# Optimization experiments

Measured on AMD Instinct MI355X. Metric: run time of the kernel, lower is better.

Reference implementation:

```python
import jax, jax.numpy as jnp
import numpy as np

IN_DIM = 768
HID = 128
NUM_CLASSES = 32
N_NODES = 50000
N_EDGES = 1600000


def setup_inputs() -> dict:
    key = jax.random.key(0)
    ks = jax.random.split(key, 8)
    x = jax.random.normal(ks[0], (N_NODES, IN_DIM), dtype=jnp.float32)
    edge_index = jax.random.randint(ks[1], (2, N_EDGES), 0, N_NODES, dtype=jnp.int64)
    # GCNConv weights (PyG: linear without bias inside propagate, bias added after aggregation)
    W1 = jax.random.normal(ks[2], (IN_DIM, HID), dtype=jnp.float32) / np.sqrt(IN_DIM)
    b1 = jnp.zeros((HID,), dtype=jnp.float32)
    W2 = jax.random.normal(ks[3], (HID, HID), dtype=jnp.float32) / np.sqrt(HID)
    b2 = jnp.zeros((HID,), dtype=jnp.float32)
    Wfc = jax.random.normal(ks[4], (HID, NUM_CLASSES), dtype=jnp.float32) / np.sqrt(HID)
    bfc = jnp.zeros((NUM_CLASSES,), dtype=jnp.float32)
    return {"x": x, "edge_index": edge_index, "W1": W1, "b1": b1,
            "W2": W2, "b2": b2, "Wfc": Wfc, "bfc": bfc}


def _gcn_conv(x, src, dst, norm, W, b, num_nodes):
    # PyG GCNConv: h = x @ W; out[i] = sum_j norm_ij * h[j]; out += b
    h = x @ W                      # [N, out_dim]
    msgs = h[src] * norm[:, None]  # gather + scale, [E+N, out_dim]
    out = jax.ops.segment_sum(msgs, dst, num_segments=num_nodes)
    return out + b


def reference(x, edge_index, W1, b1, W2, b2, Wfc, bfc):
    n = x.shape[0]
    loop = jnp.arange(n, dtype=edge_index.dtype)
    src = jnp.concatenate([edge_index[0], loop])  # add self-loops
    dst = jnp.concatenate([edge_index[1], loop])
    # symmetric normalization: deg computed on destination with unit edge weights
    deg = jax.ops.segment_sum(jnp.ones_like(src, dtype=x.dtype), dst, num_segments=n)
    dinv = jnp.where(deg > 0, jax.lax.rsqrt(jnp.maximum(deg, 1.0)), 0.0)
    norm = dinv[src] * dinv[dst]  # [E+N]

    h = jax.nn.relu(_gcn_conv(x, src, dst, norm, W1, b1, n))
    h = jax.nn.relu(_gcn_conv(h, src, dst, norm, W2, b2, n))
    return h @ Wfc + bfc
```

## Files before the change

kernel.cpp:

```cpp
#include <hip/hip_runtime.h>
#include <hip/hip_bf16.h>
#include <hip/hip_fp16.h>

#define N_NODES 50000
#define IN_DIM 768
#define HID 128
#define NCLS 32
#define CHUNK 8192
#define NBUCK ((N_NODES + 255) >> 8)

typedef __attribute__((ext_vector_type(8))) short bf16x8;
typedef __attribute__((ext_vector_type(4))) float f32x4;
typedef __attribute__((ext_vector_type(4))) unsigned short u16x4;

__device__ inline void split_bf16(float x, unsigned short& hi, unsigned short& lo) {
    unsigned int u = __float_as_uint(x);
    hi = (unsigned short)(u >> 16);
    float r = x - __uint_as_float(u & 0xFFFF0000u);
    lo = (unsigned short)(__float_as_uint(r) >> 16);
}

__global__ __launch_bounds__(256) void count_bucket(const int* __restrict__ raw, int E,
                                                    int* __restrict__ hist) {
    __shared__ int cnt[NBUCK];
    bool is64 = (raw[1] == 0 && raw[3] == 0 && raw[5] == 0 && raw[7] == 0);
    int t = threadIdx.x, b = blockIdx.x;
    if (t < NBUCK) cnt[t] = 0;
    __syncthreads();
    int base = b * CHUNK;
#pragma unroll
    for (int j = 0; j < CHUNK / 256; ++j) {
        int e = base + j * 256 + t;
        if (e < E) {
            int d = is64 ? raw[2 * (E + e)] : raw[E + e];
            atomicAdd(&cnt[d >> 8], 1);
        }
    }
    __syncthreads();
    if (t < NBUCK) hist[b * NBUCK + t] = cnt[t];
}

__global__ __launch_bounds__(256) void scan_off2(const int* __restrict__ hist, int nblk,
                                                 int E, int* __restrict__ bstart,
                                                 int* __restrict__ off) {
    __shared__ int tot[256];
    int t = threadIdx.x;
    int sum = 0;
    if (t < NBUCK)
        for (int b = 0; b < nblk; ++b) sum += hist[b * NBUCK + t];
    tot[t] = (t < NBUCK) ? sum : 0;
    __syncthreads();
    for (int o = 1; o < 256; o <<= 1) {
        int v = (t >= o) ? tot[t - o] : 0;
        __syncthreads();
        tot[t] += v;
        __syncthreads();
    }
    int excl = (t == 0) ? 0 : tot[t - 1];
    if (t < NBUCK) {
        bstart[t] = excl;
        int run = excl;
        for (int b = 0; b < nblk; ++b) {
            off[b * NBUCK + t] = run;
            run += hist[b * NBUCK + t];
        }
    }
    if (t == 0) bstart[NBUCK] = E;
}

__global__ __launch_bounds__(256) void chunk_scatter(const int* __restrict__ raw, int E,
                                                     const int* __restrict__ off,
                                                     unsigned int* __restrict__ ebuf) {
    __shared__ int offl[NBUCK];
    __shared__ int cnt[NBUCK];
    bool is64 = (raw[1] == 0 && raw[3] == 0 && raw[5] == 0 && raw[7] == 0);
    int t = threadIdx.x, b = blockIdx.x;
    if (t < NBUCK) { offl[t] = off[b * NBUCK + t]; cnt[t] = 0; }
    __syncthreads();
    int base = b * CHUNK;
#pragma unroll
    for (int j = 0; j < CHUNK / 256; ++j) {
        int e = base + j * 256 + t;
        if (e < E) {
            int s, d;
            if (is64) { s = raw[2 * e]; d = raw[2 * (E + e)]; }
            else      { s = raw[e];     d = raw[E + e]; }
            int k = d >> 8;
            int r = atomicAdd(&cnt[k], 1);
            ebuf[offl[k] + r] = ((unsigned int)(d & 255) << 16) | (unsigned int)s;
        }
    }
}

__global__ __launch_bounds__(256) void bucket_fine2(const unsigned int* __restrict__ ebuf,
                                                    const int* __restrict__ bstart,
                                                    int* __restrict__ rowp,
                                                    float* __restrict__ dinv,
                                                    unsigned short* __restrict__ csr,
                                                    int n, int E) {
    __shared__ int cnt[256];
    __shared__ int pre[256];
    __shared__ int fil[256];
    int k = blockIdx.x, t = threadIdx.x;
    int base = k << 8;
    int nn = min(256, n - base);
    int es = bstart[k], ee = bstart[k + 1];
    cnt[t] = 0;
    __syncthreads();
    for (int p = es + t; p < ee; p += 256) atomicAdd(&cnt[ebuf[p] >> 16], 1);
    __syncthreads();
    pre[t] = cnt[t];
    __syncthreads();
    for (int o = 1; o < 256; o <<= 1) {
        int v = (t >= o) ? pre[t - o] : 0;
        __syncthreads();
        pre[t] += v;
        __syncthreads();
    }
    int excl = (t == 0) ? 0 : pre[t - 1];
    if (t < nn) {
        rowp[base + t] = es + excl;
        dinv[base + t] = rsqrtf((float)(cnt[t] + 1));
    }
    if (k == gridDim.x - 1 && t == 0) rowp[n] = E;
    fil[t] = es + excl;
    __syncthreads();
    for (int p = es + t; p < ee; p += 256) {
        unsigned int u = ebuf[p];
        int q = atomicAdd(&fil[u >> 16], 1);
        csr[q] = (unsigned short)(u & 0xFFFFu);
    }
}

__global__ void pack_w(const float* __restrict__ W, int K,
                       unsigned short* __restrict__ ph, unsigned short* __restrict__ pl) {
    int gid = blockIdx.x * 256 + threadIdx.x;
    int total = (K / 32) * 8 * 64;
    if (gid >= total) return;
    int l = gid & 63;
    int c0 = (gid >> 6) & 7;
    int t = gid >> 9;
    int col = c0 * 16 + (l & 15);
    int k0 = t * 32 + ((l >> 4) << 3);
    size_t base = (size_t)gid * 8;
#pragma unroll
    for (int j = 0; j < 8; ++j) {
        unsigned short h, lo;
        split_bf16(W[(size_t)(k0 + j) * 128 + col], h, lo);
        ph[base + j] = h;
        pl[base + j] = lo;
    }
}

template <bool AHALF>
__device__ inline float4 loadA4(const void* A, size_t idx) {
    if constexpr (AHALF) {
        uint2 u = *(const uint2*)((const __half*)A + idx);
        float2 f0 = __half22float2(*(__half2*)&u.x);
        float2 f1 = __half22float2(*(__half2*)&u.y);
        return make_float4(f0.x, f0.y, f1.x, f1.y);
    } else {
        return *(const float4*)((const float*)A + idx);
    }
}

template <int K, bool AHALF>
__global__ __launch_bounds__(256) void gemm_mfma2(const void* __restrict__ A,
                                                  const unsigned short* __restrict__ Bph,
                                                  const unsigned short* __restrict__ Bpl,
                                                  const float* __restrict__ dinv,
                                                  __half* __restrict__ Chalf, int M) {
    __shared__ unsigned short Ah[64][40];
    __shared__ unsigned short Al[64][40];
    int tid = threadIdx.x;
    int wid = tid >> 6, lane = tid & 63;
    int wr = wid >> 1, wc = wid & 1;
    int row0 = blockIdx.x * 64;
    int lrow = lane & 15, lk = (lane >> 4) * 8;
    const int T = K / 32;

    int sidx0 = tid, sidx1 = 256 + tid;
    int sr0 = sidx0 >> 3, sc0 = (sidx0 & 7) * 4;
    int sr1 = sidx1 >> 3, sc1 = (sidx1 & 7) * 4;
    bool v0 = (row0 + sr0) < M, v1 = (row0 + sr1) < M;
    size_t ai0 = (size_t)(row0 + sr0) * K + sc0;
    size_t ai1 = (size_t)(row0 + sr1) * K + sc1;

    float4 pre0 = make_float4(0.f, 0.f, 0.f, 0.f), pre1 = pre0;
    if (v0) pre0 = loadA4<AHALF>(A, ai0);
    if (v1) pre1 = loadA4<AHALF>(A, ai1);

    f32x4 acc[2][4] = {};
    for (int t = 0; t < T; ++t) {
        u16x4 h, lo;
        split_bf16(pre0.x, ((unsigned short*)&h)[0], ((unsigned short*)&lo)[0]);
        split_bf16(pre0.y, ((unsigned short*)&h)[1], ((unsigned short*)&lo)[1]);
        split_bf16(pre0.z, ((unsigned short*)&h)[2], ((unsigned short*)&lo)[2]);
        split_bf16(pre0.w, ((unsigned short*)&h)[3], ((unsigned short*)&lo)[3]);
        *(u16x4*)&Ah[sr0][sc0] = h;
        *(u16x4*)&Al[sr0][sc0] = lo;
        split_bf16(pre1.x, ((unsigned short*)&h)[0], ((unsigned short*)&lo)[0]);
        split_bf16(pre1.y, ((unsigned short*)&h)[1], ((unsigned short*)&lo)[1]);
        split_bf16(pre1.z, ((unsigned short*)&h)[2], ((unsigned short*)&lo)[2]);
        split_bf16(pre1.w, ((unsigned short*)&h)[3], ((unsigned short*)&lo)[3]);
        *(u16x4*)&Ah[sr1][sc1] = h;
        *(u16x4*)&Al[sr1][sc1] = lo;
        __syncthreads();
        if (t + 1 < T) {
            pre0 = make_float4(0.f, 0.f, 0.f, 0.f); pre1 = pre0;
            if (v0) pre0 = loadA4<AHALF>(A, ai0 + (size_t)(t + 1) * 32);
            if (v1) pre1 = loadA4<AHALF>(A, ai1 + (size_t)(t + 1) * 32);
        }
        bf16x8 ah[2], al[2];
#pragma unroll
        for (int m = 0; m < 2; ++m) {
            int r = wr * 32 + m * 16 + lrow;
            ah[m] = *(const bf16x8*)&Ah[r][lk];
            al[m] = *(const bf16x8*)&Al[r][lk];
        }
        bf16x8 bh[4], bl[4];
#pragma unroll
        for (int n = 0; n < 4; ++n) {
            size_t boff = ((size_t)(t * 8 + wc * 4 + n) * 64 + lane) * 8;
            bh[n] = *(const bf16x8*)&Bph[boff];
            bl[n] = *(const bf16x8*)&Bpl[boff];
        }
#pragma unroll
        for (int m = 0; m < 2; ++m)
#pragma unroll
            for (int n = 0; n < 4; ++n) {
                acc[m][n] = __builtin_amdgcn_mfma_f32_16x16x32_bf16(ah[m], bh[n], acc[m][n], 0, 0, 0);
                acc[m][n] = __builtin_amdgcn_mfma_f32_16x16x32_bf16(al[m], bh[n], acc[m][n], 0, 0, 0);
                acc[m][n] = __builtin_amdgcn_mfma_f32_16x16x32_bf16(ah[m], bl[n], acc[m][n], 0, 0, 0);
            }
        __syncthreads();
    }
#pragma unroll
    for (int m = 0; m < 2; ++m) {
        int rbase = row0 + wr * 32 + m * 16 + (lane >> 4) * 4;
#pragma unroll
        for (int n = 0; n < 4; ++n) {
            int col = wc * 64 + n * 16 + lrow;
#pragma unroll
            for (int j = 0; j < 4; ++j) {
                int r = rbase + j;
                if (r < M) Chalf[(size_t)r * 128 + col] = __float2half(dinv[r] * acc[m][n][j]);
            }
        }
    }
}

__global__ __launch_bounds__(256) void aggregate5(const __half* __restrict__ ht,
                                                  const int* __restrict__ rowp,
                                                  const unsigned short* __restrict__ csr,
                                                  const float* __restrict__ dinv,
                                                  const float* __restrict__ bias,
                                                  __half* __restrict__ outh, int n) {
    int wid = threadIdx.x >> 6, lane = threadIdx.x & 63;
    int i = blockIdx.x * 4 + wid;
    if (i >= n) return;
    const __half2* h2 = (const __half2*)ht;
    float di = dinv[i];
    float2 acc = __half22float2(h2[(size_t)i * 64 + lane]);
    int b = rowp[i], e = rowp[i + 1];
    int p = b;
    for (; p + 16 <= e; p += 16) {
        int s[16]; float2 v[16];
#pragma unroll
        for (int q = 0; q < 16; ++q) s[q] = csr[p + q];
#pragma unroll
        for (int q = 0; q < 16; ++q) v[q] = __half22float2(h2[(size_t)s[q] * 64 + lane]);
#pragma unroll
        for (int q = 0; q < 16; ++q) { acc.x += v[q].x; acc.y += v[q].y; }
    }
    for (; p + 4 <= e; p += 4) {
        int s[4]; float2 v[4];
#pragma unroll
        for (int q = 0; q < 4; ++q) s[q] = csr[p + q];
#pragma unroll
        for (int q = 0; q < 4; ++q) v[q] = __half22float2(h2[(size_t)s[q] * 64 + lane]);
#pragma unroll
        for (int q = 0; q < 4; ++q) { acc.x += v[q].x; acc.y += v[q].y; }
    }
    for (; p < e; ++p) {
        float2 v = __half22float2(h2[(size_t)csr[p] * 64 + lane]);
        acc.x += v.x;
        acc.y += v.y;
    }
    float2 bb = ((const float2*)bias)[lane];
    __half2 o = __floats2half2_rn(fmaxf(di * acc.x + bb.x, 0.f),
                                  fmaxf(di * acc.y + bb.y, 0.f));
    ((__half2*)outh)[(size_t)i * 64 + lane] = o;
}

__global__ __launch_bounds__(256) void fc_out(const __half* __restrict__ h,
                                              const float* __restrict__ W,
                                              const float* __restrict__ b,
                                              float* __restrict__ out, int n) {
    __shared__ float Ws[HID * NCLS];
    __shared__ float Hs[8][HID];
    int tid = threadIdx.x;
#pragma unroll
    for (int l = 0; l < 16; ++l) Ws[l * 256 + tid] = W[l * 256 + tid];
    int row0 = blockIdx.x * 8;
#pragma unroll
    for (int l = 0; l < 4; ++l) {
        int idx = l * 256 + tid;
        int r = idx >> 7, c = idx & 127;
        int gr = row0 + r;
        Hs[r][c] = (gr < n) ? __half2float(h[(size_t)gr * HID + c]) : 0.f;
    }
    __syncthreads();
    int r = tid >> 5, c = tid & 31;
    float acc = b[c];
#pragma unroll
    for (int k = 0; k < HID; ++k) acc += Hs[r][k] * Ws[k * NCLS + c];
    int gr = row0 + r;
    if (gr < n) out[(size_t)gr * NCLS + c] = acc;
}

extern "C" void kernel_launch(void* const* d_in, const int* in_sizes, int n_in,
                              void* d_out, int out_size, void* d_ws, size_t ws_size,
                              hipStream_t stream) {
    const float* x   = (const float*)d_in[0];
    const int*   eid = (const int*)d_in[1];
    const float* W1  = (const float*)d_in[2];
    const float* b1  = (const float*)d_in[3];
    const float* W2  = (const float*)d_in[4];
    const float* b2  = (const float*)d_in[5];
    const float* Wfc = (const float*)d_in[6];
    const float* bfc = (const float*)d_in[7];
    float* out = (float*)d_out;

    const int N = N_NODES;
    const int E = in_sizes[1] / 2;
    const int NBLK = (E + CHUNK - 1) / CHUNK;

    auto align = [](size_t v) { return (v + 255) & ~(size_t)255; };
    char* w = (char*)d_ws;
    size_t off = 0;
    int* rowp = (int*)(w + off);           off = align(off + (size_t)(N + 1) * 4);
    float* dinv = (float*)(w + off);       off = align(off + (size_t)N * 4);
    unsigned short* csr = (unsigned short*)(w + off); off = align(off + (size_t)E * 2);
    unsigned int* ebuf = (unsigned int*)(w + off);    off = align(off + (size_t)E * 4);
    int* bstart = (int*)(w + off);         off = align(off + (size_t)(NBUCK + 1) * 4);
    int* hist = (int*)(w + off);           off = align(off + (size_t)NBLK * NBUCK * 4);
    int* offs = (int*)(w + off);           off = align(off + (size_t)NBLK * NBUCK * 4);
    unsigned short* W1ph = (unsigned short*)(w + off); off = align(off + (size_t)128 * IN_DIM * 2);
    unsigned short* W1pl = (unsigned short*)(w + off); off = align(off + (size_t)128 * IN_DIM * 2);
    unsigned short* W2ph = (unsigned short*)(w + off); off = align(off + (size_t)128 * HID * 2);
    unsigned short* W2pl = (unsigned short*)(w + off); off = align(off + (size_t)128 * HID * 2);
    __half* ht1 = (__half*)(w + off);      off = align(off + (size_t)N * HID * 2);
    __half* ht2 = (__half*)(w + off);      off = align(off + (size_t)N * HID * 2);
    __half* h1r = (__half*)(w + off);      off = align(off + (size_t)N * HID * 2);
    __half* h2r = (__half*)(w + off);      off = align(off + (size_t)N * HID * 2);

    count_bucket<<<NBLK, 256, 0, stream>>>(eid, E, hist);
    scan_off2<<<1, 256, 0, stream>>>(hist, NBLK, E, bstart, offs);
    chunk_scatter<<<NBLK, 256, 0, stream>>>(eid, E, offs, ebuf);
    bucket_fine2<<<NBUCK, 256, 0, stream>>>(ebuf, bstart, rowp, dinv, csr, N, E);

    pack_w<<<((IN_DIM / 32) * 8 * 64 + 255) / 256, 256, 0, stream>>>(W1, IN_DIM, W1ph, W1pl);
    pack_w<<<((HID / 32) * 8 * 64 + 255) / 256, 256, 0, stream>>>(W2, HID, W2ph, W2pl);

    int gb = (N + 63) / 64;
    int ab = (N + 3) / 4;
    gemm_mfma2<IN_DIM, false><<<gb, 256, 0, stream>>>(x, W1ph, W1pl, dinv, ht1, N);
    aggregate5<<<ab, 256, 0, stream>>>(ht1, rowp, csr, dinv, b1, h1r, N);
    gemm_mfma2<HID, true><<<gb, 256, 0, stream>>>(h1r, W2ph, W2pl, dinv, ht2, N);
    aggregate5<<<ab, 256, 0, stream>>>(ht2, rowp, csr, dinv, b2, h2r, N);
    fc_out<<<(N + 7) / 8, 256, 0, stream>>>(h2r, Wfc, bfc, out, N);
}
```

Baseline: 280.6 us.

## Double-buffer GEMM LDS tiles and widen K step to 64

The MFMA GEMM now stages A tiles in two LDS buffers with a K step of 64 instead of 32. The next tile's split-bf16 conversion and store go into the alternate buffer after the MFMAs, so only one barrier per iteration is needed instead of two. This aims to overlap global loads with compute and halve the synchronisation count, in exchange for four times the LDS footprint and more prefetch registers, which may lower occupancy.

```diff
diff --git a/kernel.cpp b/kernel.cpp
--- a/kernel.cpp
+++ b/kernel.cpp
@@ -165,75 +165,100 @@
 }
 
 template <int K, bool AHALF>
-__global__ __launch_bounds__(256) void gemm_mfma2(const void* __restrict__ A,
+__global__ __launch_bounds__(256) void gemm_mfma4(const void* __restrict__ A,
                                                   const unsigned short* __restrict__ Bph,
                                                   const unsigned short* __restrict__ Bpl,
                                                   const float* __restrict__ dinv,
                                                   __half* __restrict__ Chalf, int M) {
-    __shared__ unsigned short Ah[64][40];
-    __shared__ unsigned short Al[64][40];
+    __shared__ unsigned short Ah[2][64][72];
+    __shared__ unsigned short Al[2][64][72];
     int tid = threadIdx.x;
     int wid = tid >> 6, lane = tid & 63;
     int wr = wid >> 1, wc = wid & 1;
     int row0 = blockIdx.x * 64;
-    int lrow = lane & 15, lk = (lane >> 4) * 8;
-    const int T = K / 32;
-
-    int sidx0 = tid, sidx1 = 256 + tid;
-    int sr0 = sidx0 >> 3, sc0 = (sidx0 & 7) * 4;
-    int sr1 = sidx1 >> 3, sc1 = (sidx1 & 7) * 4;
-    bool v0 = (row0 + sr0) < M, v1 = (row0 + sr1) < M;
-    size_t ai0 = (size_t)(row0 + sr0) * K + sc0;
-    size_t ai1 = (size_t)(row0 + sr1) * K + sc1;
-
-    float4 pre0 = make_float4(0.f, 0.f, 0.f, 0.f), pre1 = pre0;
-    if (v0) pre0 = loadA4<AHALF>(A, ai0);
-    if (v1) pre1 = loadA4<AHALF>(A, ai1);
+    int lrow = lane & 15;
+    const int T = K / 64;
+
+    int sr[4], sc[4];
+    bool vv[4];
+    size_t abase[4];
+#pragma unroll
+    for (int q = 0; q < 4; ++q) {
+        int idx = q * 256 + tid;
+        sr[q] = idx >> 4;
+        sc[q] = (idx & 15) * 4;
+        vv[q] = (row0 + sr[q]) < M;
+        abase[q] = (size_t)(row0 + sr[q]) * K + sc[q];
+    }
+
+    float4 pre[4];
+#pragma unroll
+    for (int q = 0; q < 4; ++q)
+        pre[q] = vv[q] ? loadA4<AHALF>(A, abase[q]) : make_float4(0.f, 0.f, 0.f, 0.f);
+
+#pragma unroll
+    for (int q = 0; q < 4; ++q) {
+        u16x4 h, lo;
+        split_bf16(pre[q].x, ((unsigned short*)&h)[0], ((unsigned short*)&lo)[0]);
+        split_bf16(pre[q].y, ((unsigned short*)&h)[1], ((unsigned short*)&lo)[1]);
+        split_bf16(pre[q].z, ((unsigned short*)&h)[2], ((unsigned short*)&lo)[2]);
+        split_bf16(pre[q].w, ((unsigned short*)&h)[3], ((unsigned short*)&lo)[3]);
+        *(u16x4*)&Ah[0][sr[q]][sc[q]] = h;
+        *(u16x4*)&Al[0][sr[q]][sc[q]] = lo;
+    }
+    __syncthreads();
 
     f32x4 acc[2][4] = {};
+    int cur = 0;
     for (int t = 0; t < T; ++t) {
-        u16x4 h, lo;
-        split_bf16(pre0.x, ((unsigned short*)&h)[0], ((unsigned short*)&lo)[0]);
-        split_bf16(pre0.y, ((unsigned short*)&h)[1], ((unsigned short*)&lo)[1]);
-        split_bf16(pre0.z, ((unsigned short*)&h)[2], ((unsigned short*)&lo)[2]);
-        split_bf16(pre0.w, ((unsigned short*)&h)[3], ((unsigned short*)&lo)[3]);
-        *(u16x4*)&Ah[sr0][sc0] = h;
-        *(u16x4*)&Al[sr0][sc0] = lo;
-        split_bf16(pre1.x, ((unsigned short*)&h)[0], ((unsigned short*)&lo)[0]);
-        split_bf16(pre1.y, ((unsigned short*)&h)[1], ((unsigned short*)&lo)[1]);
-        split_bf16(pre1.z, ((unsigned short*)&h)[2], ((unsigned short*)&lo)[2]);
-        split_bf16(pre1.w, ((unsigned short*)&h)[3], ((unsigned short*)&lo)[3]);
-        *(u16x4*)&Ah[sr1][sc1] = h;
-        *(u16x4*)&Al[sr1][sc1] = lo;
-        __syncthreads();
         if (t + 1 < T) {
-            pre0 = make_float4(0.f, 0.f, 0.f, 0.f); pre1 = pre0;
-            if (v0) pre0 = loadA4<AHALF>(A, ai0 + (size_t)(t + 1) * 32);
-            if (v1) pre1 = loadA4<AHALF>(A, ai1 + (size_t)(t + 1) * 32);
-        }
-        bf16x8 ah[2], al[2];
-#pragma unroll
-        for (int m = 0; m < 2; ++m) {
-            int r = wr * 32 + m * 16 + lrow;
-            ah[m] = *(const bf16x8*)&Ah[r][lk];
-            al[m] = *(const bf16x8*)&Al[r][lk];
-        }
-        bf16x8 bh[4], bl[4];
-#pragma unroll
-        for (int n = 0; n < 4; ++n) {
-            size_t boff = ((size_t)(t * 8 + wc * 4 + n) * 64 + lane) * 8;
-            bh[n] = *(const bf16x8*)&Bph[boff];
-            bl[n] = *(const bf16x8*)&Bpl[boff];
-        }
-#pragma unroll
-        for (int m = 0; m < 2; ++m)
+#pragma unroll
+            for (int q = 0; q < 4; ++q)
+                pre[q] = vv[q] ? loadA4<AHALF>(A, abase[q] + (size_t)(t + 1) * 64)
+                               : make_float4(0.f, 0.f, 0.f, 0.f);
+        }
+#pragma unroll
+        for (int ks = 0; ks < 2; ++ks) {
+            int lk2 = ks * 32 + (lane >> 4) * 8;
+            bf16x8 ah[2], al[2];
+#pragma unroll
+            for (int m = 0; m < 2; ++m) {
+                int r = wr * 32 + m * 16 + lrow;
+                ah[m] = *(const bf16x8*)&Ah[cur][r][lk2];
+                al[m] = *(const bf16x8*)&Al[cur][r][lk2];
+            }
+            int t32 = t * 2 + ks;
+            bf16x8 bh[4], bl[4];
 #pragma unroll
             for (int n = 0; n < 4; ++n) {
-                acc[m][n] = __builtin_amdgcn_mfma_f32_16x16x32_bf16(ah[m], bh[n], acc[m][n], 0, 0, 0);
-                acc[m][n] = __builtin_amdgcn_mfma_f32_16x16x32_bf16(al[m], bh[n], acc[m][n], 0, 0, 0);
-                acc[m][n] = __builtin_amdgcn_mfma_f32_16x16x32_bf16(ah[m], bl[n], acc[m][n], 0, 0, 0);
+                size_t boff = ((size_t)(t32 * 8 + wc * 4 + n) * 64 + lane) * 8;
+                bh[n] = *(const bf16x8*)&Bph[boff];
+                bl[n] = *(const bf16x8*)&Bpl[boff];
             }
-        __syncthreads();
+#pragma unroll
+            for (int m = 0; m < 2; ++m)
+#pragma unroll
+                for (int n = 0; n < 4; ++n) {
+                    acc[m][n] = __builtin_amdgcn_mfma_f32_16x16x32_bf16(ah[m], bh[n], acc[m][n], 0, 0, 0);
+                    acc[m][n] = __builtin_amdgcn_mfma_f32_16x16x32_bf16(al[m], bh[n], acc[m][n], 0, 0, 0);
+                    acc[m][n] = __builtin_amdgcn_mfma_f32_16x16x32_bf16(ah[m], bl[n], acc[m][n], 0, 0, 0);
+                }
+        }
+        if (t + 1 < T) {
+            int nxt = cur ^ 1;
+#pragma unroll
+            for (int q = 0; q < 4; ++q) {
+                u16x4 h, lo;
+                split_bf16(pre[q].x, ((unsigned short*)&h)[0], ((unsigned short*)&lo)[0]);
+                split_bf16(pre[q].y, ((unsigned short*)&h)[1], ((unsigned short*)&lo)[1]);
+                split_bf16(pre[q].z, ((unsigned short*)&h)[2], ((unsigned short*)&lo)[2]);
+                split_bf16(pre[q].w, ((unsigned short*)&h)[3], ((unsigned short*)&lo)[3]);
+                *(u16x4*)&Ah[nxt][sr[q]][sc[q]] = h;
+                *(u16x4*)&Al[nxt][sr[q]][sc[q]] = lo;
+            }
+            __syncthreads();
+            cur = nxt;
+        }
     }
 #pragma unroll
     for (int m = 0; m < 2; ++m) {
@@ -365,9 +390,9 @@
 
     int gb = (N + 63) / 64;
     int ab = (N + 3) / 4;
-    gemm_mfma2<IN_DIM, false><<<gb, 256, 0, stream>>>(x, W1ph, W1pl, dinv, ht1, N);
+    gemm_mfma4<IN_DIM, false><<<gb, 256, 0, stream>>>(x, W1ph, W1pl, dinv, ht1, N);
     aggregate5<<<ab, 256, 0, stream>>>(ht1, rowp, csr, dinv, b1, h1r, N);
-    gemm_mfma2<HID, true><<<gb, 256, 0, stream>>>(h1r, W2ph, W2pl, dinv, ht2, N);
+    gemm_mfma4<HID, true><<<gb, 256, 0, stream>>>(h1r, W2ph, W2pl, dinv, ht2, N);
     aggregate5<<<ab, 256, 0, stream>>>(ht2, rowp, csr, dinv, b2, h2r, N);
     fc_out<<<(N + 7) / 8, 256, 0, stream>>>(h2r, Wfc, bfc, out, N);
 }
```

Result: slower. 300.7 us (+7.2%).
